# Optimization experiments

Measured on AMD Instinct MI355X. Metric: run time of the kernel, lower is better.

## Reference

```python
import jax, jax.numpy as jnp
import numpy as np

N = 50000      # nodes
E = 800000     # edges (avg degree 16)
C_IN = 256
C_OUT = 256
H = 4
D = C_OUT // H  # 64
NEG_SLOPE = 0.2


def setup_inputs() -> dict:
    key = jax.random.key(0)
    ks = jax.random.split(key, 12)
    glorot = lambda k, shape: jax.random.uniform(k, shape, jnp.float32, -1.0, 1.0) * np.sqrt(6.0 / (shape[0] + shape[1]))
    return {
        "x": jax.random.normal(ks[0], (N, C_IN), jnp.float32),
        "src": jax.random.randint(ks[1], (E,), 0, N, jnp.int32),
        "dst": jax.random.randint(ks[2], (E,), 0, N, jnp.int32),
        "Wl": glorot(ks[3], (C_IN, C_OUT)),
        "bl": jnp.zeros((C_OUT,), jnp.float32),
        "Wr": glorot(ks[4], (C_IN, C_OUT)),
        "br": jnp.zeros((C_OUT,), jnp.float32),
        "Wv": glorot(ks[5], (C_IN, C_OUT)),
        "bv": jnp.zeros((C_OUT,), jnp.float32),
        "att_l": jax.random.normal(ks[6], (1, H, D), jnp.float32) * 0.1,
        "att_r": jax.random.normal(ks[7], (1, H, D), jnp.float32) * 0.1,
    }


def reference(x, src, dst, Wl, bl, Wr, br, Wv, bv, att_l, att_r):
    # lambda_policy=None, gcn_mode=False -> lmbda = lmbda2 = 1.0
    n = x.shape[0]
    sl = ((x @ Wl + bl).reshape(n, H, D) * att_l).sum(-1, keepdims=True)  # [N,H,1]
    sr = ((x @ Wr + br).reshape(n, H, D) * att_r).sum(-1, keepdims=True)  # [N,H,1]
    xv = (x @ Wv + bv).reshape(n, H, D)                                    # [N,H,D]

    # --- convolve branch: average scores over in-neighborhood (incl. self) ---
    hlr = jnp.concatenate([sl, sr], axis=1)                   # [N,2H,1]
    conv = jax.ops.segment_sum(hlr[src], dst, num_segments=n)  # sum_{u->v} hsrc[u]
    deg = jax.ops.segment_sum(jnp.ones((src.shape[0],), x.dtype), dst, num_segments=n)
    agg = (hlr + conv) / (1.0 + deg[:, None, None])            # [N,2H,1]
    sl, sr = agg[:, :H], agg[:, H:]

    # --- edge attention: gather-add-leakyrelu, segment softmax over dst ---
    e = jax.nn.leaky_relu(sl[src] + sr[dst], NEG_SLOPE)        # [E,H,1]
    emax = jax.ops.segment_max(e, dst, num_segments=n)
    emax = jnp.where(jnp.isfinite(emax), emax, 0.0)
    ex = jnp.exp(e - emax[dst])
    denom = jax.ops.segment_sum(ex, dst, num_segments=n)
    a = ex / jnp.maximum(denom[dst], 1e-16)                    # [E,H,1]

    # --- weighted message aggregation ---
    out = jax.ops.segment_sum(xv[src] * a, dst, num_segments=n)  # [N,H,D]
    return out
```

## Files before the change

kernel.cpp:

```cpp
#include <hip/hip_runtime.h>

#define C_IN 256
#define C_OUT 256
#define NH 4
#define HD 64
#define NEG_SLOPE 0.2f

typedef _Float16 half8 __attribute__((ext_vector_type(8)));
typedef _Float16 half4v __attribute__((ext_vector_type(4)));
typedef float floatx4 __attribute__((ext_vector_type(4)));

__global__ void make_eff_w(const float* __restrict__ Wl, const float* __restrict__ Wr,
                           const float* __restrict__ bl, const float* __restrict__ br,
                           const float* __restrict__ attl, const float* __restrict__ attr,
                           float* __restrict__ Ws, float* __restrict__ bs)
{
    int c = blockIdx.x;
    int t = threadIdx.x;
    int h = t >> 6, d = t & 63;
    float al = attl[t], ar = attr[t];
    float vl, vr;
    if (c < C_IN) { vl = Wl[c * C_OUT + t] * al; vr = Wr[c * C_OUT + t] * ar; }
    else          { vl = bl[t] * al;             vr = br[t] * ar; }
#pragma unroll
    for (int off = 32; off >= 1; off >>= 1) {
        vl += __shfl_xor(vl, off, 64);
        vr += __shfl_xor(vr, off, 64);
    }
    if (d == 0) {
        if (c < C_IN) { Ws[c * 8 + h] = vl; Ws[c * 8 + 4 + h] = vr; }
        else          { bs[h] = vl;         bs[4 + h] = vr; }
    }
}

__global__ void transpose_w(const float* __restrict__ Wv, _Float16* __restrict__ WvT)
{
    int idx = blockIdx.x * 256 + threadIdx.x;
    int n = idx >> 8, k = idx & 255;
    WvT[n * 256 + k] = (_Float16)Wv[k * 256 + n];
}

__global__ __launch_bounds__(256) void node_scores(const float* __restrict__ x,
    const float* __restrict__ Ws, const float* __restrict__ bs,
    float* __restrict__ s, int N)
{
    int lane = threadIdx.x & 63, wid = threadIdx.x >> 6;
    float w[4][8];
#pragma unroll
    for (int i = 0; i < 4; ++i)
#pragma unroll
        for (int jq = 0; jq < 2; ++jq) {
            float4 v = *(const float4*)(Ws + (4 * lane + i) * 8 + jq * 4);
            w[i][jq * 4 + 0] = v.x; w[i][jq * 4 + 1] = v.y;
            w[i][jq * 4 + 2] = v.z; w[i][jq * 4 + 3] = v.w;
        }
    float b0[8];
#pragma unroll
    for (int j = 0; j < 8; ++j) b0[j] = bs[j];

    int wglob = blockIdx.x * 4 + wid;
    int nwaves = gridDim.x * 4;
    for (int n = wglob; n < N; n += nwaves) {
        float4 xv4 = *(const float4*)(x + (size_t)n * 256 + 4 * lane);
        float acc[8];
#pragma unroll
        for (int j = 0; j < 8; ++j)
            acc[j] = xv4.x * w[0][j] + xv4.y * w[1][j] + xv4.z * w[2][j] + xv4.w * w[3][j];
#pragma unroll
        for (int off = 32; off >= 1; off >>= 1)
#pragma unroll
            for (int j = 0; j < 8; ++j) acc[j] += __shfl_xor(acc[j], off, 64);
        if (lane == 0) {
            *(float4*)(s + (size_t)n * 8)     = make_float4(acc[0] + b0[0], acc[1] + b0[1], acc[2] + b0[2], acc[3] + b0[3]);
            *(float4*)(s + (size_t)n * 8 + 4) = make_float4(acc[4] + b0[4], acc[5] + b0[5], acc[6] + b0[6], acc[7] + b0[7]);
        }
    }
}

__global__ __launch_bounds__(256) void gemm_xv(const float* __restrict__ x,
    const _Float16* __restrict__ WvT, const float* __restrict__ bv,
    _Float16* __restrict__ xv, int M)
{
    __shared__ __align__(16) _Float16 As[128][40];
    __shared__ __align__(16) _Float16 Bs[128][40];
    int tid = threadIdx.x;
    int wid = tid >> 6, lane = tid & 63;
    int quad = lane >> 4, r16 = lane & 15;
    int m0 = blockIdx.x * 128, n0 = blockIdx.y * 128;

    floatx4 acc[2][8];
#pragma unroll
    for (int i = 0; i < 2; ++i)
#pragma unroll
        for (int j = 0; j < 8; ++j) acc[i][j] = (floatx4){0.f, 0.f, 0.f, 0.f};

    int arow = tid >> 3, af4 = tid & 7;
    int brow = tid >> 2, bg  = tid & 3;

    for (int k0 = 0; k0 < 256; k0 += 32) {
#pragma unroll
        for (int p = 0; p < 4; ++p) {
            int rr = arow + p * 32;
            int gm = m0 + rr;
            float4 v = make_float4(0.f, 0.f, 0.f, 0.f);
            if (gm < M) v = *(const float4*)(x + (size_t)gm * 256 + k0 + af4 * 4);
            half4v tmp;
            tmp[0] = (_Float16)v.x; tmp[1] = (_Float16)v.y;
            tmp[2] = (_Float16)v.z; tmp[3] = (_Float16)v.w;
            *(half4v*)&As[rr][af4 * 4] = tmp;
        }
#pragma unroll
        for (int p = 0; p < 2; ++p) {
            int nr = brow + p * 64;
            *(float4*)&Bs[nr][bg * 8] = *(const float4*)(WvT + (size_t)(n0 + nr) * 256 + k0 + bg * 8);
        }
        __syncthreads();
        half8 a[2], b[8];
#pragma unroll
        for (int rg = 0; rg < 2; ++rg)
            a[rg] = *(const half8*)&As[wid * 32 + rg * 16 + r16][quad * 8];
#pragma unroll
        for (int cg = 0; cg < 8; ++cg)
            b[cg] = *(const half8*)&Bs[cg * 16 + r16][quad * 8];
#pragma unroll
        for (int rg = 0; rg < 2; ++rg)
#pragma unroll
            for (int cg = 0; cg < 8; ++cg)
                acc[rg][cg] = __builtin_amdgcn_mfma_f32_16x16x32_f16(a[rg], b[cg], acc[rg][cg], 0, 0, 0);
        __syncthreads();
    }
#pragma unroll
    for (int rg = 0; rg < 2; ++rg) {
        int rbase = m0 + wid * 32 + rg * 16 + quad * 4;
#pragma unroll
        for (int cg = 0; cg < 8; ++cg) {
            int gcol = n0 + cg * 16 + r16;
            float bias = bv[gcol];
#pragma unroll
            for (int rr = 0; rr < 4; ++rr) {
                int grow = rbase + rr;
                if (grow < M)
                    xv[(size_t)grow * 256 + gcol] = (_Float16)(acc[rg][cg][rr] + bias);
            }
        }
    }
}

__global__ void deg_kernel(const int* __restrict__ dst, int* __restrict__ deg, int E)
{
    int i = blockIdx.x * 256 + threadIdx.x;
    if (i < E) atomicAdd(&deg[dst[i]], 1);
}

__global__ void scan_part(const int* __restrict__ deg, int* __restrict__ partials,
                          int N, int chunk)
{
    __shared__ int sd[256];
    int b = blockIdx.x, t = threadIdx.x;
    int idx = b * chunk + t;
    int v = (t < chunk && idx < N) ? deg[idx] : 0;
    sd[t] = v; __syncthreads();
    for (int off = 128; off >= 1; off >>= 1) {
        if (t < off) sd[t] += sd[t + off];
        __syncthreads();
    }
    if (t == 0) partials[b] = sd[0];
}

__global__ void scan_partials(const int* __restrict__ partials, int* __restrict__ pscan)
{
    __shared__ int sd[256];
    int t = threadIdx.x;
    int v = partials[t];
    sd[t] = v; __syncthreads();
    for (int off = 1; off < 256; off <<= 1) {
        int x = (t >= off) ? sd[t - off] : 0;
        __syncthreads();
        sd[t] += x;
        __syncthreads();
    }
    pscan[t] = sd[t] - v;
}

__global__ void scan_final(const int* __restrict__ deg, const int* __restrict__ pscan,
                           int* __restrict__ offs, int N, int chunk)
{
    __shared__ int sd[256];
    int b = blockIdx.x, t = threadIdx.x;
    int idx = b * chunk + t;
    int v = (t < chunk && idx < N) ? deg[idx] : 0;
    sd[t] = v; __syncthreads();
    for (int off = 1; off < 256; off <<= 1) {
        int x = (t >= off) ? sd[t - off] : 0;
        __syncthreads();
        sd[t] += x;
        __syncthreads();
    }
    int incl = sd[t], excl = incl - v;
    int base = pscan[b];
    if (t < chunk && idx < N) offs[idx] = base + excl;
    if (idx == N - 1) offs[N] = base + incl;
}

__global__ void scatter_kernel(const int* __restrict__ src, const int* __restrict__ dst,
                               const int* __restrict__ offs, int* __restrict__ cursor,
                               int* __restrict__ csr_src, int E)
{
    int i = blockIdx.x * 256 + threadIdx.x;
    if (i < E) {
        int d = dst[i];
        int p = offs[d] + atomicAdd(&cursor[d], 1);
        csr_src[p] = src[i];
    }
}

__global__ void agg_kernel(const float* __restrict__ s, const int* __restrict__ csr_src,
                           const int* __restrict__ offs, const int* __restrict__ deg,
                           float* __restrict__ aggl, float* __restrict__ aggr, int N)
{
    int gid = blockIdx.x * 256 + threadIdx.x;
    int n = gid >> 3, c = gid & 7;
    if (n >= N) return;
    int off = offs[n], dg = deg[n];
    float acc = s[(size_t)n * 8 + c];
    int i = 0;
    for (; i + 4 <= dg; i += 4) {
        int p0 = csr_src[off + i];
        int p1 = csr_src[off + i + 1];
        int p2 = csr_src[off + i + 2];
        int p3 = csr_src[off + i + 3];
        float v0 = s[(size_t)p0 * 8 + c];
        float v1 = s[(size_t)p1 * 8 + c];
        float v2 = s[(size_t)p2 * 8 + c];
        float v3 = s[(size_t)p3 * 8 + c];
        acc += (v0 + v1) + (v2 + v3);
    }
    for (; i < dg; ++i) acc += s[(size_t)csr_src[off + i] * 8 + c];
    acc *= 1.0f / (1.0f + (float)dg);
    if (c < 4) aggl[(size_t)n * 4 + c]     = acc;
    else       aggr[(size_t)n * 4 + c - 4] = acc;
}

template<int SZ>
__device__ __forceinline__ void gather_sub(int cs, float w, int base, int grp, int lof,
    const _Float16* __restrict__ xv,
    float& o0, float& o1, float& o2, float& o3)
{
    half4v hv[SZ];
#pragma unroll
    for (int j = 0; j < SZ; ++j) {
        int sidx = __builtin_amdgcn_readlane(cs, base + j);
        hv[j] = *(const half4v*)(xv + (((unsigned)sidx << 8) + lof));
    }
#pragma unroll
    for (int j = 0; j < SZ; ++j) {
        float wv = __shfl(w, grp + base + j, 64);
        o0 += wv * (float)hv[j][0];
        o1 += wv * (float)hv[j][1];
        o2 += wv * (float)hv[j][2];
        o3 += wv * (float)hv[j][3];
    }
}

__device__ __forceinline__ void do_chunk(int cs, float w, int cnt, int grp, int lof,
    const _Float16* __restrict__ xv,
    float& o0, float& o1, float& o2, float& o3)
{
    if (cnt == 16) { gather_sub<16>(cs, w, 0, grp, lof, xv, o0, o1, o2, o3); return; }
    int b = 0;
    if (cnt & 8) { gather_sub<8>(cs, w, b, grp, lof, xv, o0, o1, o2, o3); b += 8; }
    if (cnt & 4) { gather_sub<4>(cs, w, b, grp, lof, xv, o0, o1, o2, o3); b += 4; }
    if (cnt & 2) { gather_sub<2>(cs, w, b, grp, lof, xv, o0, o1, o2, o3); b += 2; }
    if (cnt & 1) { gather_sub<1>(cs, w, b, grp, lof, xv, o0, o1, o2, o3); }
}

__global__ __launch_bounds__(256) void attn_out(const float* __restrict__ aggl,
    const float* __restrict__ aggr, const int* __restrict__ csr_src,
    const int* __restrict__ offs, const int* __restrict__ deg,
    const _Float16* __restrict__ xv, float* __restrict__ out, int N)
{
    int wid = threadIdx.x >> 6, lane = threadIdx.x & 63;
    int n = blockIdx.x * 4 + wid;
    if (n >= N) return;
    int myhead = lane >> 4, myedge = lane & 15, grp = lane & 48;
    int lof = lane << 2;
    int off = offs[n], dg = deg[n];
    const int* cb = csr_src + off;
    float ar = aggr[(unsigned)(n * 4 + myhead)];

    float o0 = 0.f, o1 = 0.f, o2 = 0.f, o3 = 0.f;

    int cs0 = 0, cs1 = 0, cs2 = 0, cs3 = 0;
    int e1 = myedge + 16, e2 = myedge + 32, e3 = myedge + 48;
    if (myedge < dg) cs0 = cb[myedge];
    if (e1 < dg)     cs1 = cb[e1];
    if (e2 < dg)     cs2 = cb[e2];
    if (e3 < dg)     cs3 = cb[e3];
    float a0 = 0.f, a1 = 0.f, a2 = 0.f, a3 = 0.f;
    if (myedge < dg) a0 = aggl[(unsigned)((cs0 << 2) + myhead)];
    if (e1 < dg)     a1 = aggl[(unsigned)((cs1 << 2) + myhead)];
    if (e2 < dg)     a2 = aggl[(unsigned)((cs2 << 2) + myhead)];
    if (e3 < dg)     a3 = aggl[(unsigned)((cs3 << 2) + myhead)];
    float w0 = 0.f, w1 = 0.f, w2 = 0.f, w3 = 0.f;
    if (myedge < dg) { float e = a0 + ar; e = (e > 0.f) ? e : NEG_SLOPE * e; w0 = __expf(e); }
    if (e1 < dg)     { float e = a1 + ar; e = (e > 0.f) ? e : NEG_SLOPE * e; w1 = __expf(e); }
    if (e2 < dg)     { float e = a2 + ar; e = (e > 0.f) ? e : NEG_SLOPE * e; w2 = __expf(e); }
    if (e3 < dg)     { float e = a3 + ar; e = (e > 0.f) ? e : NEG_SLOPE * e; w3 = __expf(e); }
    float denom = w0; denom += w1; denom += w2; denom += w3;

    int c0 = dg < 16 ? dg : 16;
    do_chunk(cs0, w0, c0, grp, lof, xv, o0, o1, o2, o3);
    if (dg > 16) {
        int c1 = dg - 16 < 16 ? dg - 16 : 16;
        do_chunk(cs1, w1, c1, grp, lof, xv, o0, o1, o2, o3);
    }
    if (dg > 32) {
        int c2 = dg - 32 < 16 ? dg - 32 : 16;
        do_chunk(cs2, w2, c2, grp, lof, xv, o0, o1, o2, o3);
    }
    if (dg > 48) {
        int c3 = dg - 48 < 16 ? dg - 48 : 16;
        do_chunk(cs3, w3, c3, grp, lof, xv, o0, o1, o2, o3);
    }
    for (int b = 64; b < dg; b += 16) {
        int cs = 0; float w = 0.f;
        if (b + myedge < dg) {
            cs = cb[b + myedge];
            float e = aggl[(unsigned)((cs << 2) + myhead)] + ar;
            e = (e > 0.f) ? e : NEG_SLOPE * e;
            w = __expf(e);
        }
        denom += w;
        int cnt = dg - b < 16 ? dg - b : 16;
        do_chunk(cs, w, cnt, grp, lof, xv, o0, o1, o2, o3);
    }

#pragma unroll
    for (int o = 1; o <= 8; o <<= 1) denom += __shfl_xor(denom, o, 64);
    float inv = 1.0f / fmaxf(denom, 1e-16f);
    floatx4 res = {o0 * inv, o1 * inv, o2 * inv, o3 * inv};
    __builtin_nontemporal_store(res, (floatx4*)(out + (size_t)n * 256 + lof));
}

extern "C" void kernel_launch(void* const* d_in, const int* in_sizes, int n_in,
                              void* d_out, int out_size, void* d_ws, size_t ws_size,
                              hipStream_t stream)
{
    const float* x    = (const float*)d_in[0];
    const int*   src  = (const int*)d_in[1];
    const int*   dst  = (const int*)d_in[2];
    const float* Wl   = (const float*)d_in[3];
    const float* bl   = (const float*)d_in[4];
    const float* Wr   = (const float*)d_in[5];
    const float* br   = (const float*)d_in[6];
    const float* Wv   = (const float*)d_in[7];
    const float* bv   = (const float*)d_in[8];
    const float* attl = (const float*)d_in[9];
    const float* attr = (const float*)d_in[10];
    float* out = (float*)d_out;

    int N = in_sizes[0] / C_IN;
    int E = in_sizes[1];

    char* p = (char*)d_ws;
    auto alloc = [&](size_t bytes) -> void* {
        uintptr_t q = (uintptr_t)p;
        q = (q + 255) & ~(uintptr_t)255;
        p = (char*)(q + bytes);
        return (void*)q;
    };
    float* Ws     = (float*)alloc((size_t)C_IN * 8 * sizeof(float));
    float* bs     = (float*)alloc(8 * sizeof(float));
    float* s      = (float*)alloc((size_t)N * 8 * sizeof(float));
    float* aggl   = (float*)alloc((size_t)N * 4 * sizeof(float));
    float* aggr   = (float*)alloc((size_t)N * 4 * sizeof(float));
    int* deg      = (int*)alloc((size_t)N * sizeof(int));
    int* offs     = (int*)alloc((size_t)(N + 1) * sizeof(int));
    int* cursor   = (int*)alloc((size_t)N * sizeof(int));
    int* partials = (int*)alloc(256 * sizeof(int));
    int* pscan    = (int*)alloc(256 * sizeof(int));
    int* csr_src  = (int*)alloc((size_t)E * sizeof(int));
    _Float16* WvT = (_Float16*)alloc((size_t)C_IN * C_OUT * sizeof(_Float16));
    _Float16* xv  = (_Float16*)alloc((size_t)N * C_OUT * sizeof(_Float16));

    hipMemsetAsync(deg, 0, (size_t)N * sizeof(int), stream);
    hipMemsetAsync(cursor, 0, (size_t)N * sizeof(int), stream);

    make_eff_w<<<C_IN + 1, 256, 0, stream>>>(Wl, Wr, bl, br, attl, attr, Ws, bs);
    transpose_w<<<(C_IN * C_OUT) / 256, 256, 0, stream>>>(Wv, WvT);
    node_scores<<<768, 256, 0, stream>>>(x, Ws, bs, s, N);
    gemm_xv<<<dim3((N + 127) / 128, C_OUT / 128), 256, 0, stream>>>(x, WvT, bv, xv, N);
    deg_kernel<<<(E + 255) / 256, 256, 0, stream>>>(dst, deg, E);
    int chunk = (N + 255) / 256;
    scan_part<<<256, 256, 0, stream>>>(deg, partials, N, chunk);
    scan_partials<<<1, 256, 0, stream>>>(partials, pscan);
    scan_final<<<256, 256, 0, stream>>>(deg, pscan, offs, N, chunk);
    scatter_kernel<<<(E + 255) / 256, 256, 0, stream>>>(src, dst, offs, cursor, csr_src, E);
    agg_kernel<<<(N * 8 + 255) / 256, 256, 0, stream>>>(s, csr_src, offs, deg, aggl, aggr, N);
    attn_out<<<(N + 3) / 4, 256, 0, stream>>>(aggl, aggr, csr_src, offs, deg, xv, out, N);
}
```

Before: 347.0 us.

## Fuse node score projection into value GEMM and vectorize edge atomics

Removes the separate node_scores kernel and computes the 8 per-node attention scores inside gemm_xv, in blocks with blockIdx.y==0, reusing the fp32 x tile already loaded for the MFMA GEMM. This avoids a second full pass over x (about 51 MB) and one launch. It adds FMA work and registers to half the GEMM blocks, which creates load imbalance and may lower occupancy. Separately, deg_kernel and scatter_kernel now handle four edges per thread with int4 loads.

```diff
diff --git a/kernel.cpp b/kernel.cpp
--- a/kernel.cpp
+++ b/kernel.cpp
@@ -40,46 +40,10 @@
     WvT[n * 256 + k] = (_Float16)Wv[k * 256 + n];
 }
 
-__global__ __launch_bounds__(256) void node_scores(const float* __restrict__ x,
-    const float* __restrict__ Ws, const float* __restrict__ bs,
-    float* __restrict__ s, int N)
-{
-    int lane = threadIdx.x & 63, wid = threadIdx.x >> 6;
-    float w[4][8];
-#pragma unroll
-    for (int i = 0; i < 4; ++i)
-#pragma unroll
-        for (int jq = 0; jq < 2; ++jq) {
-            float4 v = *(const float4*)(Ws + (4 * lane + i) * 8 + jq * 4);
-            w[i][jq * 4 + 0] = v.x; w[i][jq * 4 + 1] = v.y;
-            w[i][jq * 4 + 2] = v.z; w[i][jq * 4 + 3] = v.w;
-        }
-    float b0[8];
-#pragma unroll
-    for (int j = 0; j < 8; ++j) b0[j] = bs[j];
-
-    int wglob = blockIdx.x * 4 + wid;
-    int nwaves = gridDim.x * 4;
-    for (int n = wglob; n < N; n += nwaves) {
-        float4 xv4 = *(const float4*)(x + (size_t)n * 256 + 4 * lane);
-        float acc[8];
-#pragma unroll
-        for (int j = 0; j < 8; ++j)
-            acc[j] = xv4.x * w[0][j] + xv4.y * w[1][j] + xv4.z * w[2][j] + xv4.w * w[3][j];
-#pragma unroll
-        for (int off = 32; off >= 1; off >>= 1)
-#pragma unroll
-            for (int j = 0; j < 8; ++j) acc[j] += __shfl_xor(acc[j], off, 64);
-        if (lane == 0) {
-            *(float4*)(s + (size_t)n * 8)     = make_float4(acc[0] + b0[0], acc[1] + b0[1], acc[2] + b0[2], acc[3] + b0[3]);
-            *(float4*)(s + (size_t)n * 8 + 4) = make_float4(acc[4] + b0[4], acc[5] + b0[5], acc[6] + b0[6], acc[7] + b0[7]);
-        }
-    }
-}
-
 __global__ __launch_bounds__(256) void gemm_xv(const float* __restrict__ x,
     const _Float16* __restrict__ WvT, const float* __restrict__ bv,
-    _Float16* __restrict__ xv, int M)
+    const float* __restrict__ Ws, const float* __restrict__ bs,
+    _Float16* __restrict__ xv, float* __restrict__ s, int M)
 {
     __shared__ __align__(16) _Float16 As[128][40];
     __shared__ __align__(16) _Float16 Bs[128][40];
@@ -87,6 +51,7 @@
     int wid = tid >> 6, lane = tid & 63;
     int quad = lane >> 4, r16 = lane & 15;
     int m0 = blockIdx.x * 128, n0 = blockIdx.y * 128;
+    bool do_s = (blockIdx.y == 0);
 
     floatx4 acc[2][8];
 #pragma unroll
@@ -97,7 +62,23 @@
     int arow = tid >> 3, af4 = tid & 7;
     int brow = tid >> 2, bg  = tid & 3;
 
+    float sacc[4][8];
+#pragma unroll
+    for (int p = 0; p < 4; ++p)
+#pragma unroll
+        for (int j = 0; j < 8; ++j) sacc[p][j] = 0.f;
+
     for (int k0 = 0; k0 < 256; k0 += 32) {
+        float w8[4][8];
+        if (do_s) {
+#pragma unroll
+            for (int q = 0; q < 4; ++q) {
+                const float4* wr = (const float4*)(Ws + (size_t)(k0 + af4 * 4 + q) * 8);
+                float4 wa = wr[0], wb = wr[1];
+                w8[q][0] = wa.x; w8[q][1] = wa.y; w8[q][2] = wa.z; w8[q][3] = wa.w;
+                w8[q][4] = wb.x; w8[q][5] = wb.y; w8[q][6] = wb.z; w8[q][7] = wb.w;
+            }
+        }
 #pragma unroll
         for (int p = 0; p < 4; ++p) {
             int rr = arow + p * 32;
@@ -108,6 +89,14 @@
             tmp[0] = (_Float16)v.x; tmp[1] = (_Float16)v.y;
             tmp[2] = (_Float16)v.z; tmp[3] = (_Float16)v.w;
             *(half4v*)&As[rr][af4 * 4] = tmp;
+            if (do_s) {
+                float xq[4] = {v.x, v.y, v.z, v.w};
+#pragma unroll
+                for (int q = 0; q < 4; ++q)
+#pragma unroll
+                    for (int j = 0; j < 8; ++j)
+                        sacc[p][j] += xq[q] * w8[q][j];
+            }
         }
 #pragma unroll
         for (int p = 0; p < 2; ++p) {
@@ -129,6 +118,26 @@
                 acc[rg][cg] = __builtin_amdgcn_mfma_f32_16x16x32_f16(a[rg], b[cg], acc[rg][cg], 0, 0, 0);
         __syncthreads();
     }
+
+    if (do_s) {
+        float b0[8];
+#pragma unroll
+        for (int j = 0; j < 8; ++j) b0[j] = bs[j];
+#pragma unroll
+        for (int p = 0; p < 4; ++p) {
+#pragma unroll
+            for (int o = 1; o <= 4; o <<= 1)
+#pragma unroll
+                for (int j = 0; j < 8; ++j)
+                    sacc[p][j] += __shfl_xor(sacc[p][j], o, 64);
+            int gm = m0 + arow + p * 32;
+            if (af4 == 0 && gm < M) {
+                *(float4*)(s + (size_t)gm * 8)     = make_float4(sacc[p][0] + b0[0], sacc[p][1] + b0[1], sacc[p][2] + b0[2], sacc[p][3] + b0[3]);
+                *(float4*)(s + (size_t)gm * 8 + 4) = make_float4(sacc[p][4] + b0[4], sacc[p][5] + b0[5], sacc[p][6] + b0[6], sacc[p][7] + b0[7]);
+            }
+        }
+    }
+
 #pragma unroll
     for (int rg = 0; rg < 2; ++rg) {
         int rbase = m0 + wid * 32 + rg * 16 + quad * 4;
@@ -149,7 +158,17 @@
 __global__ void deg_kernel(const int* __restrict__ dst, int* __restrict__ deg, int E)
 {
     int i = blockIdx.x * 256 + threadIdx.x;
-    if (i < E) atomicAdd(&deg[dst[i]], 1);
+    int base = i * 4;
+    if (base >= E) return;
+    if (base + 4 <= E) {
+        int4 d = *(const int4*)(dst + base);
+        atomicAdd(&deg[d.x], 1);
+        atomicAdd(&deg[d.y], 1);
+        atomicAdd(&deg[d.z], 1);
+        atomicAdd(&deg[d.w], 1);
+    } else {
+        for (int k = base; k < E; ++k) atomicAdd(&deg[dst[k]], 1);
+    }
 }
 
 __global__ void scan_part(const int* __restrict__ deg, int* __restrict__ partials,
@@ -207,10 +226,21 @@
                                int* __restrict__ csr_src, int E)
 {
     int i = blockIdx.x * 256 + threadIdx.x;
-    if (i < E) {
-        int d = dst[i];
-        int p = offs[d] + atomicAdd(&cursor[d], 1);
-        csr_src[p] = src[i];
+    int base = i * 4;
+    if (base >= E) return;
+    if (base + 4 <= E) {
+        int4 d  = *(const int4*)(dst + base);
+        int4 sv = *(const int4*)(src + base);
+        int p0 = offs[d.x] + atomicAdd(&cursor[d.x], 1); csr_src[p0] = sv.x;
+        int p1 = offs[d.y] + atomicAdd(&cursor[d.y], 1); csr_src[p1] = sv.y;
+        int p2 = offs[d.z] + atomicAdd(&cursor[d.z], 1); csr_src[p2] = sv.z;
+        int p3 = offs[d.w] + atomicAdd(&cursor[d.w], 1); csr_src[p3] = sv.w;
+    } else {
+        for (int k = base; k < E; ++k) {
+            int d = dst[k];
+            int p = offs[d] + atomicAdd(&cursor[d], 1);
+            csr_src[p] = src[k];
+        }
     }
 }
 
@@ -388,14 +418,13 @@
 
     make_eff_w<<<C_IN + 1, 256, 0, stream>>>(Wl, Wr, bl, br, attl, attr, Ws, bs);
     transpose_w<<<(C_IN * C_OUT) / 256, 256, 0, stream>>>(Wv, WvT);
-    node_scores<<<768, 256, 0, stream>>>(x, Ws, bs, s, N);
-    gemm_xv<<<dim3((N + 127) / 128, C_OUT / 128), 256, 0, stream>>>(x, WvT, bv, xv, N);
-    deg_kernel<<<(E + 255) / 256, 256, 0, stream>>>(dst, deg, E);
+    gemm_xv<<<dim3((N + 127) / 128, C_OUT / 128), 256, 0, stream>>>(x, WvT, bv, Ws, bs, xv, s, N);
+    deg_kernel<<<((E + 3) / 4 + 255) / 256, 256, 0, stream>>>(dst, deg, E);
     int chunk = (N + 255) / 256;
     scan_part<<<256, 256, 0, stream>>>(deg, partials, N, chunk);
     scan_partials<<<1, 256, 0, stream>>>(partials, pscan);
     scan_final<<<256, 256, 0, stream>>>(deg, pscan, offs, N, chunk);
-    scatter_kernel<<<(E + 255) / 256, 256, 0, stream>>>(src, dst, offs, cursor, csr_src, E);
+    scatter_kernel<<<((E + 3) / 4 + 255) / 256, 256, 0, stream>>>(src, dst, offs, cursor, csr_src, E);
     agg_kernel<<<(N * 8 + 255) / 256, 256, 0, stream>>>(s, csr_src, offs, deg, aggl, aggr, N);
     attn_out<<<(N + 3) / 4, 256, 0, stream>>>(aggl, aggr, csr_src, offs, deg, xv, out, N);
 }
```

Measured after the change: 330.8 us. 4.7% less time.
